# Kernel tuning notes

Hardware: AMD Instinct MI355X
Metric: run time of the kernel (lower is better)

The kernel has to match this reference:

```python
import jax, jax.numpy as jnp
import numpy as np

N, E, G = 8000, 32000, 256   # nodes, edges, graphs
F, H = 680, 10               # in-features, GAT heads
HF = F * H                   # 6800


def setup_inputs() -> dict:
    key = jax.random.key(0)
    ks = jax.random.split(key, 12)
    s = lambda i, shape, sc: (jax.random.normal(ks[i], shape, jnp.float32) * sc)
    x = jax.random.normal(ks[0], (N, F), jnp.float32)
    edge_index = jax.random.randint(ks[1], (2, E), 0, N)
    batch = jnp.arange(N) // (N // G)   # contiguous, every graph non-empty
    return dict(
        x=x, edge_index=edge_index, batch=batch,
        W_gat=s(2, (F, HF), 0.05), a_src=s(3, (H, F), 0.05), a_dst=s(4, (H, F), 0.05),
        b_gat=jnp.zeros((HF,), jnp.float32),
        W_gcn=s(5, (HF, HF), 0.01), b_gcn=jnp.zeros((HF,), jnp.float32),
        W1=s(6, (2 * HF, 512), 0.02), b1=jnp.zeros((512,), jnp.float32),
        W2=s(7, (512, 128), 0.05), b2=jnp.zeros((128,), jnp.float32),
        W3=s(8, (128, 64), 0.05), b3=jnp.zeros((64,), jnp.float32),
    )


def _self_loops(edge_index):
    loop = jnp.arange(N)
    return (jnp.concatenate([edge_index[0], loop]),
            jnp.concatenate([edge_index[1], loop]))


def _gat(x, src, dst, W, a_s, a_d, b):
    xh = (x @ W).reshape(N, H, F)                          # [N,H,F]
    al_s = jnp.einsum('nhf,hf->nh', xh, a_s)               # src attention logits
    al_d = jnp.einsum('nhf,hf->nh', xh, a_d)
    e = jax.nn.leaky_relu(al_s[src] + al_d[dst], 0.2)      # [Etot,H]
    m = jax.ops.segment_max(e, dst, num_segments=N)        # segment softmax over dst
    ex = jnp.exp(e - m[dst])
    z = jax.ops.segment_sum(ex, dst, num_segments=N)
    alpha = ex / (z[dst] + 1e-16)
    out = jax.ops.segment_sum(alpha[:, :, None] * xh[src], dst, num_segments=N)
    return out.reshape(N, HF) + b                          # concat heads + bias


def _gcn(x, src, dst, W, b):
    deg = jax.ops.segment_sum(jnp.ones_like(dst, jnp.float32), dst, num_segments=N)
    dinv = jax.lax.rsqrt(deg)                              # deg>=1 due to self-loops
    norm = dinv[src] * dinv[dst]
    xw = x @ W
    return jax.ops.segment_sum(norm[:, None] * xw[src], dst, num_segments=N) + b


def reference(x, edge_index, batch, W_gat, a_src, a_dst, b_gat, W_gcn, b_gcn,
              W1, b1, W2, b2, W3, b3):
    src, dst = _self_loops(edge_index)
    h = jax.nn.relu(_gat(x, src, dst, W_gat, a_src, a_dst, b_gat))  # dropout = id (eval)
    h = jax.nn.relu(_gcn(h, src, dst, W_gcn, b_gcn))
    gmp = jax.ops.segment_max(h, batch, num_segments=G)
    cnt = jax.ops.segment_sum(jnp.ones((N,), jnp.float32), batch, num_segments=G)
    gap = jax.ops.segment_sum(h, batch, num_segments=G) / cnt[:, None]
    g = jnp.concatenate([gmp, gap], axis=1)                # [G, 2*HF]
    g = jax.nn.relu(g @ W1 + b1)
    g = g @ W2 + b2
    return g @ W3 + b3                                     # [G, 64]
```

## Files before the change

kernel.cpp:

```cpp
#include <hip/hip_runtime.h>
#include <cstdint>
#include <cstddef>

#define DEVFN static __device__ __forceinline__

typedef __attribute__((ext_vector_type(8))) short short8;
typedef __attribute__((ext_vector_type(4))) float f32x4;

constexpr int NN  = 8000;
constexpr int NE  = 32000;
constexpr int ET  = NE + NN;
constexpr int NG  = 256;
constexpr int F   = 680;
constexpr int NH  = 10;
constexpr int HF  = 6800;

constexpr int MP   = 8192;
constexpr int KP1  = 704;
constexpr int NP   = 6912;
constexpr int KP2  = 6848;
constexpr int KM1P = 13632;

DEVFN unsigned short f2bf(float f) {
  unsigned u = __float_as_uint(f);
  u += 0x7fffu + ((u >> 16) & 1u);
  return (unsigned short)(u >> 16);
}
DEVFN float bf2f(unsigned short b) { return __uint_as_float(((unsigned)b) << 16); }

DEVFN int perm64(int k, int r) {
  return (((k >> 3) ^ (r & 7)) << 3) | (k & 7);
}

DEVFN void gload16(const void* g, void* l) {
  __builtin_amdgcn_global_load_lds(
      (const __attribute__((address_space(1))) unsigned int*)g,
      (__attribute__((address_space(3))) unsigned int*)l, 16, 0, 0);
}

DEVFN f32x4 mfma_16x16x32_bf16(short8 a, short8 b, f32x4 c) {
  asm("v_mfma_f32_16x16x32_bf16 %0, %1, %2, %0" : "+v"(c) : "v"(a), "v"(b));
  return c;
}

template<int OUT_MODE, bool BIAS, bool RELU>
__global__ __launch_bounds__(512, 2) void gemm256(
    const unsigned short* __restrict__ A, const unsigned short* __restrict__ BT,
    void* __restrict__ C, const float* __restrict__ bias,
    int K, int cstride, int nvalid, int Mt, int KC) {
  __shared__ alignas(16) char Lds[131072];
  const int tid = threadIdx.x;
  const int wave = tid >> 6, lane = tid & 63;
  const int wm = wave >> 2, wn = wave & 3;
  const int g4 = lane >> 4, l15 = lane & 15;
  const int xorc = l15 & 7;
  const int brow = (wn & 1) * 64;

  const int nwg = gridDim.x, orig = blockIdx.x;
  const int qx = nwg >> 3, r8 = nwg & 7;
  const int xcd = orig & 7, loc = orig >> 3;
  const int wg = (xcd < r8 ? xcd * (qx + 1) : r8 * (qx + 1) + (xcd - r8) * qx) + loc;
  const int bm = wg % Mt, bn = wg / Mt;

  const int NTt = K >> 6;
  const int kb = blockIdx.z * KC;
  const int NT = min(KC, NTt - kb);
  const unsigned short* Ag = A + (size_t)bm * 256 * K + (size_t)kb * 64;
  const unsigned short* Bg = BT + (size_t)bn * 256 * K + (size_t)kb * 64;

  const int srow = tid >> 3;
  const int schk = (tid & 7) * 8;

  auto stageHalf = [&](const unsigned short* G, int t, int op, int h) {
    char* base = Lds + ((((t & 1) << 2) | (op << 1) | h) << 14) + (wave << 10);
    const unsigned short* src = G + (size_t)(h * 128 + srow) * K + (size_t)t * 64 + schk;
    gload16(src, base);
    gload16(src + (size_t)64 * K, base + 8192);
  };

  const char* Ab0 = Lds + (((0 << 2) | (0 << 1) | wm) << 14);
  const char* Ab1 = Lds + (((1 << 2) | (0 << 1) | wm) << 14);
  const char* Bb0 = Lds + (((0 << 2) | (1 << 1) | (wn >> 1)) << 14);
  const char* Bb1 = Lds + (((1 << 2) | (1 << 1) | (wn >> 1)) << 14);

  f32x4 acc[8][4];
#pragma unroll
  for (int i = 0; i < 8; i++)
#pragma unroll
    for (int j = 0; j < 4; j++) acc[i][j] = (f32x4){0.f, 0.f, 0.f, 0.f};

  short8 aR[4][2], b0[2][2], b1[2][2];

#define READ_A(BASE, QM) do {                                                   \
  _Pragma("unroll") for (int i2 = 0; i2 < 4; ++i2)                              \
  _Pragma("unroll") for (int ks = 0; ks < 2; ++ks)                              \
    aR[i2][ks] = *(const short8*)((BASE) + ((QM) * 64 + i2 * 16 + l15) * 128    \
                                  + ((((ks << 2) | g4) ^ xorc) << 4));          \
} while (0)

#define READ_B(BASE, QN, DST) do {                                              \
  _Pragma("unroll") for (int j2 = 0; j2 < 2; ++j2)                              \
  _Pragma("unroll") for (int ks = 0; ks < 2; ++ks)                              \
    DST[j2][ks] = *(const short8*)((BASE) + (brow + (QN) * 32 + j2 * 16 + l15) * 128 \
                                   + ((((ks << 2) | g4) ^ xorc) << 4));         \
} while (0)

#define MMAQ(QM, QN, BREG) do {                                                 \
  _Pragma("unroll") for (int i2 = 0; i2 < 4; ++i2)                              \
  _Pragma("unroll") for (int j2 = 0; j2 < 2; ++j2)                              \
  _Pragma("unroll") for (int ks = 0; ks < 2; ++ks)                              \
    acc[(QM) * 4 + i2][(QN) * 2 + j2] =                                         \
        mfma_16x16x32_bf16(aR[i2][ks], BREG[j2][ks], acc[(QM) * 4 + i2][(QN) * 2 + j2]); \
} while (0)

  if (NT > 0) {
    stageHalf(Ag, 0, 0, 0); stageHalf(Ag, 0, 0, 1);
    stageHalf(Bg, 0, 1, 0); stageHalf(Bg, 0, 1, 1);
  }
  if (NT > 1) {
    stageHalf(Ag, 1, 0, 0); stageHalf(Ag, 1, 0, 1);
    stageHalf(Bg, 1, 1, 0); stageHalf(Bg, 1, 1, 1);
    asm volatile("s_waitcnt vmcnt(8)" ::: "memory");
  } else {
    asm volatile("s_waitcnt vmcnt(0)" ::: "memory");
  }
  __builtin_amdgcn_s_barrier();

  for (int t = 0; t < NT; ++t) {
    const char* Ac = (t & 1) ? Ab1 : Ab0;
    const char* Bc = (t & 1) ? Bb1 : Bb0;
    const bool pf = (t + 2 < NT);

    READ_A(Ac, 0);
    READ_B(Bc, 0, b0);
    __builtin_amdgcn_s_barrier();
    asm volatile("s_waitcnt lgkmcnt(0)" ::: "memory");
    __builtin_amdgcn_s_setprio(1);
    MMAQ(0, 0, b0);
    __builtin_amdgcn_s_setprio(0);
    __builtin_amdgcn_s_barrier();

    READ_B(Bc, 1, b1);
    __builtin_amdgcn_s_barrier();
    asm volatile("s_waitcnt lgkmcnt(0)" ::: "memory");
    __builtin_amdgcn_s_setprio(1);
    MMAQ(0, 1, b1);
    __builtin_amdgcn_s_setprio(0);
    __builtin_amdgcn_s_barrier();

    READ_A(Ac, 1);
    if (pf) { stageHalf(Bg, t + 2, 1, 0); stageHalf(Bg, t + 2, 1, 1); }
    __builtin_amdgcn_s_barrier();
    asm volatile("s_waitcnt lgkmcnt(0)" ::: "memory");
    __builtin_amdgcn_s_setprio(1);
    MMAQ(1, 1, b1);
    __builtin_amdgcn_s_setprio(0);
    __builtin_amdgcn_s_barrier();

    if (pf) {
      stageHalf(Ag, t + 2, 0, 0); stageHalf(Ag, t + 2, 0, 1);
      asm volatile("s_waitcnt vmcnt(8)" ::: "memory");
    } else {
      asm volatile("s_waitcnt vmcnt(0)" ::: "memory");
    }
    __builtin_amdgcn_s_barrier();
    __builtin_amdgcn_s_setprio(1);
    MMAQ(1, 0, b0);
    __builtin_amdgcn_s_setprio(0);
    __builtin_amdgcn_s_barrier();
  }

#undef READ_A
#undef READ_B
#undef MMAQ

  const int m0 = bm * 256 + wm * 128;
  const int n0 = bn * 256 + wn * 64;
  const int rb = g4 * 4;
#pragma unroll
  for (int i = 0; i < 8; i++) {
#pragma unroll
    for (int j = 0; j < 4; j++) {
      int c = n0 + j * 16 + l15;
      if (c >= nvalid) continue;
      float bv = BIAS ? bias[c] : 0.f;
#pragma unroll
      for (int tt = 0; tt < 4; tt++) {
        int r = m0 + i * 16 + rb + tt;
        float v = acc[i][j][tt] + bv;
        if (RELU) v = fmaxf(v, 0.f);
        if (OUT_MODE == 0) {
          ((float*)C)[(size_t)r * cstride + c] = v;
        } else if (OUT_MODE == 1) {
          ((unsigned short*)C)[(size_t)r * cstride + c] = f2bf(v);
        } else if (OUT_MODE == 2) {
          int pos = (c & ~63) + perm64(c & 63, r);
          ((unsigned short*)C)[(size_t)r * cstride + pos] = f2bf(v);
        } else {
          ((float*)C)[(size_t)blockIdx.z * (Mt * 256) * cstride + (size_t)r * cstride + c] = v;
        }
      }
    }
  }
}

template<bool RELU>
__global__ void finish_kernel(const float* __restrict__ acc, const float* __restrict__ bias,
                              unsigned short* __restrict__ out, int S, int M, int N) {
  int idx = blockIdx.x * 256 + threadIdx.x;
  if (idx >= M * N) return;
  int r = idx / N, c = idx - r * N;
  float s = bias[c];
  for (int k = 0; k < S; k++) s += acc[(size_t)k * M * N + (size_t)r * N + c];
  if (RELU) s = fmaxf(s, 0.f);
  out[(size_t)r * N + (c & ~63) + perm64(c & 63, r)] = f2bf(s);
}

__global__ void conv_x_kernel(const float* __restrict__ x, unsigned short* __restrict__ out) {
  int idx = blockIdx.x * 256 + threadIdx.x;
  constexpr int GR = KP1 / 4;
  if (idx >= MP * GR) return;
  int row = idx / GR, k = (idx - row * GR) * 4;
  unsigned short v[4] = {0, 0, 0, 0};
  if (row < NN && k < F) {
    const float* p = x + (size_t)row * F + k;
    v[0] = f2bf(p[0]); v[1] = f2bf(p[1]); v[2] = f2bf(p[2]); v[3] = f2bf(p[3]);
  }
  int pos = (k & ~63) + perm64(k & 63, row);
  uint2 pk;
  pk.x = (unsigned)v[0] | ((unsigned)v[1] << 16);
  pk.y = (unsigned)v[2] | ((unsigned)v[3] << 16);
  *(uint2*)&out[(size_t)row * KP1 + pos] = pk;
}

__global__ void convT_kernel(const float* __restrict__ in, unsigned short* __restrict__ out,
                             int K, int N, int KPad, int NPad) {
  __shared__ float tile[32][33];
  int n0 = blockIdx.x * 32, k0 = blockIdx.y * 32;
  int tx = threadIdx.x, ty = threadIdx.y;
#pragma unroll
  for (int i = 0; i < 4; i++) {
    int k = k0 + ty + i * 8, n = n0 + tx;
    tile[ty + i * 8][tx] = (k < K && n < N) ? in[(size_t)k * N + n] : 0.f;
  }
  __syncthreads();
#pragma unroll
  for (int i = 0; i < 4; i++) {
    int n = n0 + ty + i * 8, k = k0 + tx;
    if (n < NPad && k < KPad) {
      int pos = (k & ~63) + perm64(k & 63, n);
      out[(size_t)n * KPad + pos] = f2bf(tile[tx][ty + i * 8]);
    }
  }
}

__global__ void logits_kernel(const unsigned short* __restrict__ xh,
                              const float* __restrict__ a_src, const float* __restrict__ a_dst,
                              float* __restrict__ al_s, float* __restrict__ al_d) {
  int wid = blockIdx.x * 4 + (threadIdx.x >> 6);
  int lane = threadIdx.x & 63;
  int n = wid / NH, h = wid - n * NH;
  if (n >= NN) return;
  const unsigned short* row = xh + (size_t)n * NP + h * F;
  const float* as = a_src + h * F;
  const float* ad = a_dst + h * F;
  float ss = 0.f, sd = 0.f;
  for (int f0 = lane; f0 < F; f0 += 64) {
    float v = bf2f(row[f0]);
    ss += v * as[f0]; sd += v * ad[f0];
  }
#pragma unroll
  for (int o = 32; o > 0; o >>= 1) { ss += __shfl_down(ss, o); sd += __shfl_down(sd, o); }
  if (lane == 0) { al_s[wid] = ss; al_d[wid] = sd; }
}

__global__ void edge_count_kernel(const int* __restrict__ ei, int* __restrict__ deg) {
  int e = blockIdx.x * 256 + threadIdx.x;
  if (e >= ET) return;
  int d = (e < NE) ? ei[NE + e] : (e - NE);
  atomicAdd(&deg[d], 1);
}

__global__ void scan_kernel(const int* __restrict__ deg, int* __restrict__ rs,
                            int* __restrict__ cursor) {
  __shared__ int part[1024];
  int t = threadIdx.x;
  int base = t * 8, s = 0, loc[8];
#pragma unroll
  for (int i = 0; i < 8; i++) { loc[i] = s; int idx = base + i; s += (idx < NN) ? deg[idx] : 0; }
  part[t] = s;
  __syncthreads();
  for (int off = 1; off < 1024; off <<= 1) {
    int v = (t >= off) ? part[t - off] : 0;
    __syncthreads();
    part[t] += v;
    __syncthreads();
  }
  int pre = (t > 0) ? part[t - 1] : 0;
#pragma unroll
  for (int i = 0; i < 8; i++) {
    int idx = base + i;
    if (idx <= NN) { rs[idx] = pre + loc[i]; cursor[idx] = pre + loc[i]; }
  }
}

__global__ void edge_fill_kernel(const int* __restrict__ ei, int* __restrict__ cursor,
                                 int* __restrict__ eidx) {
  int e = blockIdx.x * 256 + threadIdx.x;
  if (e >= ET) return;
  int d = (e < NE) ? ei[NE + e] : (e - NE);
  int pos = atomicAdd(&cursor[d], 1);
  eidx[pos] = e;
}

__global__ void dinv_kernel(const int* __restrict__ deg, float* __restrict__ dinv) {
  int n = blockIdx.x * 256 + threadIdx.x;
  if (n < NN) dinv[n] = rsqrtf((float)max(deg[n], 1));
}

__global__ void alpha_kernel(const int* __restrict__ ei, const int* __restrict__ rs,
                             const int* __restrict__ eidx, const float* __restrict__ al_s,
                             const float* __restrict__ al_d, float* __restrict__ alpha) {
  int w = blockIdx.x * 256 + threadIdx.x;
  if (w >= NN * NH) return;
  int n = w / NH, h = w - n * NH;
  int s0 = rs[n], s1 = rs[n + 1];
  float ad = al_d[w];
  float m = -3.0e38f;
  for (int i = s0; i < s1; i++) {
    int e = eidx[i]; int s = (e < NE) ? ei[e] : (e - NE);
    float x = al_s[s * NH + h] + ad;
    x = (x > 0.f) ? x : 0.2f * x;
    m = fmaxf(m, x);
  }
  float z = 0.f;
  for (int i = s0; i < s1; i++) {
    int e = eidx[i]; int s = (e < NE) ? ei[e] : (e - NE);
    float x = al_s[s * NH + h] + ad;
    x = (x > 0.f) ? x : 0.2f * x;
    float ex = __expf(x - m);
    alpha[(size_t)i * NH + h] = ex;
    z += ex;
  }
  float inv = 1.f / (z + 1e-16f);
  for (int i = s0; i < s1; i++) alpha[(size_t)i * NH + h] *= inv;
}

__global__ void gat_agg_kernel(const unsigned short* __restrict__ xh, const int* __restrict__ ei,
                               const int* __restrict__ rs, const int* __restrict__ eidx,
                               const float* __restrict__ alpha, const float* __restrict__ bgat,
                               unsigned short* __restrict__ hbf) {
  int n = blockIdx.x, t = threadIdx.x;
  int s0 = rs[n], s1 = rs[n + 1];
  for (int c4 = t; c4 < KP2 / 4; c4 += 256) {
    int c = c4 * 4;
    int pos = (c & ~63) + perm64(c & 63, n);
    if (c >= HF) {
      *(uint2*)&hbf[(size_t)n * KP2 + pos] = make_uint2(0u, 0u);
      continue;
    }
    int h = c / F;
    float a0 = 0.f, a1 = 0.f, a2 = 0.f, a3 = 0.f;
    for (int i = s0; i < s1; i++) {
      int e = eidx[i]; int s = (e < NE) ? ei[e] : (e - NE);
      float al = alpha[(size_t)i * NH + h];
      uint2 r = *(const uint2*)&xh[(size_t)s * NP + c];
      a0 += al * bf2f((unsigned short)(r.x & 0xffff));
      a1 += al * bf2f((unsigned short)(r.x >> 16));
      a2 += al * bf2f((unsigned short)(r.y & 0xffff));
      a3 += al * bf2f((unsigned short)(r.y >> 16));
    }
    a0 = fmaxf(a0 + bgat[c], 0.f);     a1 = fmaxf(a1 + bgat[c + 1], 0.f);
    a2 = fmaxf(a2 + bgat[c + 2], 0.f); a3 = fmaxf(a3 + bgat[c + 3], 0.f);
    uint2 pk;
    pk.x = (unsigned)f2bf(a0) | ((unsigned)f2bf(a1) << 16);
    pk.y = (unsigned)f2bf(a2) | ((unsigned)f2bf(a3) << 16);
    *(uint2*)&hbf[(size_t)n * KP2 + pos] = pk;
  }
}

__global__ void gcn_agg_kernel(const unsigned short* __restrict__ xw, const int* __restrict__ ei,
                               const int* __restrict__ rs, const int* __restrict__ eidx,
                               const float* __restrict__ dinv, const float* __restrict__ bgcn,
                               unsigned short* __restrict__ h2) {
  int n = blockIdx.x, t = threadIdx.x;
  int s0 = rs[n], s1 = rs[n + 1];
  float dn = dinv[n];
  for (int c4 = t; c4 < HF / 4; c4 += 256) {
    int c = c4 * 4;
    float a0 = 0.f, a1 = 0.f, a2 = 0.f, a3 = 0.f;
    for (int i = s0; i < s1; i++) {
      int e = eidx[i]; int s = (e < NE) ? ei[e] : (e - NE);
      float w = dinv[s] * dn;
      uint2 r = *(const uint2*)&xw[(size_t)s * NP + c];
      a0 += w * bf2f((unsigned short)(r.x & 0xffff));
      a1 += w * bf2f((unsigned short)(r.x >> 16));
      a2 += w * bf2f((unsigned short)(r.y & 0xffff));
      a3 += w * bf2f((unsigned short)(r.y >> 16));
    }
    a0 = fmaxf(a0 + bgcn[c], 0.f);     a1 = fmaxf(a1 + bgcn[c + 1], 0.f);
    a2 = fmaxf(a2 + bgcn[c + 2], 0.f); a3 = fmaxf(a3 + bgcn[c + 3], 0.f);
    uint2 pk;
    pk.x = (unsigned)f2bf(a0) | ((unsigned)f2bf(a1) << 16);
    pk.y = (unsigned)f2bf(a2) | ((unsigned)f2bf(a3) << 16);
    *(uint2*)&h2[(size_t)n * KP2 + c] = pk;
  }
}

__global__ void pool_init_kernel(int* gstart, int* gend, int* gcnt) {
  int g = threadIdx.x;
  gstart[g] = 0x7fffffff; gend[g] = 0; gcnt[g] = 0;
}
__global__ void pool_scan_kernel(const int* __restrict__ batch, int* gstart, int* gend, int* gcnt) {
  int n = blockIdx.x * 256 + threadIdx.x;
  if (n >= NN) return;
  int b = batch[n];
  if (b >= 0 && b < NG) {
    atomicMin(&gstart[b], n);
    atomicMax(&gend[b], n + 1);
    atomicAdd(&gcnt[b], 1);
  }
}
__global__ void pool_kernel(const unsigned short* __restrict__ h2, const int* __restrict__ batch,
                            const int* __restrict__ gstart, const int* __restrict__ gend,
                            const int* __restrict__ gcnt, unsigned short* __restrict__ gbf) {
  int g = blockIdx.x, t = threadIdx.x;
  int s = gstart[g], e = gend[g];
  float cnt = (float)max(gcnt[g], 1);
  for (int c = t; c < HF; c += 256) {
    float vmax = -3.0e38f, vsum = 0.f;
    for (int n = s; n < e; n++) {
      if (batch[n] != g) continue;
      float v = bf2f(h2[(size_t)n * KP2 + c]);
      vmax = fmaxf(vmax, v);
      vsum += v;
    }
    int c1 = c, c2 = HF + c;
    gbf[(size_t)g * KM1P + (c1 & ~63) + perm64(c1 & 63, g)] = f2bf(vmax);
    gbf[(size_t)g * KM1P + (c2 & ~63) + perm64(c2 & 63, g)] = f2bf(vsum / cnt);
  }
}

extern "C" void kernel_launch(void* const* d_in, const int* in_sizes, int n_in,
                              void* d_out, int out_size, void* d_ws, size_t ws_size,
                              hipStream_t stream) {
  (void)in_sizes; (void)n_in; (void)out_size; (void)ws_size;
  const float* x     = (const float*)d_in[0];
  const int*   ei    = (const int*)d_in[1];
  const int*   batch = (const int*)d_in[2];
  const float* W_gat = (const float*)d_in[3];
  const float* a_src = (const float*)d_in[4];
  const float* a_dst = (const float*)d_in[5];
  const float* b_gat = (const float*)d_in[6];
  const float* W_gcn = (const float*)d_in[7];
  const float* b_gcn = (const float*)d_in[8];
  const float* W1    = (const float*)d_in[9];
  const float* b1    = (const float*)d_in[10];
  const float* W2    = (const float*)d_in[11];
  const float* b2    = (const float*)d_in[12];
  const float* W3    = (const float*)d_in[13];
  const float* b3    = (const float*)d_in[14];
  float* out = (float*)d_out;

  char* ws = (char*)d_ws;
  size_t off = 0;
  auto alloc = [&](size_t bytes) -> void* {
    void* p = ws + off;
    off += (bytes + 255) & ~(size_t)255;
    return p;
  };
  unsigned short* bufA  = (unsigned short*)alloc((size_t)MP * NP * 2);
  unsigned short* bufB  = (unsigned short*)alloc((size_t)MP * KP2 * 2);
  unsigned short* wgcnT = (unsigned short*)alloc((size_t)NP * KP2 * 2);
  unsigned short* xbf   = (unsigned short*)alloc((size_t)MP * KP1 * 2);
  unsigned short* wgatT = (unsigned short*)alloc((size_t)NP * KP1 * 2);
  unsigned short* w1T   = (unsigned short*)alloc((size_t)512 * KM1P * 2);
  unsigned short* gbf   = (unsigned short*)alloc((size_t)NG * KM1P * 2);
  unsigned short* w2T   = (unsigned short*)alloc((size_t)256 * 512 * 2);
  unsigned short* w3T   = (unsigned short*)alloc((size_t)256 * 128 * 2);
  unsigned short* g1bf  = (unsigned short*)alloc((size_t)NG * 512 * 2);
  unsigned short* g2bf  = (unsigned short*)alloc((size_t)NG * 128 * 2);
  float* accf  = (float*)alloc((size_t)8 * 256 * 512 * 4);
  float* al_s  = (float*)alloc((size_t)NN * NH * 4);
  float* al_d  = (float*)alloc((size_t)NN * NH * 4);
  float* alpha = (float*)alloc((size_t)ET * NH * 4);
  float* dinv  = (float*)alloc((size_t)NN * 4);
  int* deg    = (int*)alloc((size_t)NN * 4);
  int* rs     = (int*)alloc((size_t)(NN + 1) * 4);
  int* cursor = (int*)alloc((size_t)(NN + 1) * 4);
  int* eidx   = (int*)alloc((size_t)ET * 4);
  int* gstart = (int*)alloc((size_t)NG * 4);
  int* gend   = (int*)alloc((size_t)NG * 4);
  int* gcnt   = (int*)alloc((size_t)NG * 4);

  constexpr int MT = MP / 256;
  constexpr int NT_ = NP / 256;

  conv_x_kernel<<<(MP * (KP1 / 4)) / 256, 256, 0, stream>>>(x, xbf);
  convT_kernel<<<dim3(NP / 32, KP1 / 32), dim3(32, 8), 0, stream>>>(W_gat, wgatT, F, HF, KP1, NP);
  convT_kernel<<<dim3(NP / 32, KP2 / 32), dim3(32, 8), 0, stream>>>(W_gcn, wgcnT, HF, HF, KP2, NP);
  convT_kernel<<<dim3(512 / 32, KM1P / 32), dim3(32, 8), 0, stream>>>(W1, w1T, 2 * HF, 512, KM1P, 512);
  convT_kernel<<<dim3(256 / 32, 512 / 32), dim3(32, 8), 0, stream>>>(W2, w2T, 512, 128, 512, 256);
  convT_kernel<<<dim3(256 / 32, 128 / 32), dim3(32, 8), 0, stream>>>(W3, w3T, 128, 64, 128, 256);
  hipMemsetAsync(deg, 0, (size_t)NN * 4, stream);
  hipMemsetAsync((char*)bufB + (size_t)NN * KP2 * 2, 0, (size_t)(MP - NN) * KP2 * 2, stream);
  hipMemsetAsync(gbf, 0, (size_t)NG * KM1P * 2, stream);

  gemm256<1, false, false><<<dim3(MT * NT_, 1, 1), 512, 0, stream>>>(
      xbf, wgatT, bufA, nullptr, KP1, NP, NP, MT, KP1 / 64);

  logits_kernel<<<(NN * NH) / 4, 256, 0, stream>>>(bufA, a_src, a_dst, al_s, al_d);

  edge_count_kernel<<<(ET + 255) / 256, 256, 0, stream>>>(ei, deg);
  scan_kernel<<<1, 1024, 0, stream>>>(deg, rs, cursor);
  edge_fill_kernel<<<(ET + 255) / 256, 256, 0, stream>>>(ei, cursor, eidx);
  dinv_kernel<<<(NN + 255) / 256, 256, 0, stream>>>(deg, dinv);

  alpha_kernel<<<(NN * NH + 255) / 256, 256, 0, stream>>>(ei, rs, eidx, al_s, al_d, alpha);

  gat_agg_kernel<<<NN, 256, 0, stream>>>(bufA, ei, rs, eidx, alpha, b_gat, bufB);

  gemm256<1, false, false><<<dim3(MT * NT_, 1, 1), 512, 0, stream>>>(
      bufB, wgcnT, bufA, nullptr, KP2, NP, NP, MT, KP2 / 64);

  gcn_agg_kernel<<<NN, 256, 0, stream>>>(bufA, ei, rs, eidx, dinv, b_gcn, bufB);

  pool_init_kernel<<<1, 256, 0, stream>>>(gstart, gend, gcnt);
  pool_scan_kernel<<<(NN + 255) / 256, 256, 0, stream>>>(batch, gstart, gend, gcnt);
  pool_kernel<<<NG, 256, 0, stream>>>(bufB, batch, gstart, gend, gcnt, gbf);

  gemm256<3, false, false><<<dim3(1 * 2, 1, 8), 512, 0, stream>>>(
      gbf, w1T, accf, nullptr, KM1P, 512, 512, 1, 27);
  finish_kernel<true><<<(256 * 512) / 256, 256, 0, stream>>>(accf, b1, g1bf, 8, 256, 512);

  gemm256<3, false, false><<<dim3(1, 1, 4), 512, 0, stream>>>(
      g1bf, w2T, accf, nullptr, 512, 128, 128, 1, 2);
  finish_kernel<false><<<(256 * 128) / 256, 256, 0, stream>>>(accf, b2, g2bf, 4, 256, 128);

  gemm256<0, true, false><<<dim3(1, 1, 1), 512, 0, stream>>>(
      g2bf, w3T, out, b3, 128, 64, 64, 1, 2);
}
```

Before: 1.688 ms.

## Cut per-iteration barriers in GEMM main loop and add XCD-aware tile mapping

Restructures the bf16 GEMM K-loop from eight barriers and explicit lgkmcnt waits per iteration down to three. Prefetches of the next B and A tiles are issued right after the barrier that follows the last reads of that buffer, so global loads overlap the remaining MFMA quads. It also replaces the generic work-group remap with a fixed swizzle for the two large GEMMs, so each XCD handles one N-column of tiles across all M tiles. Out-of-range tiles exit early. The costs are a hard-coded grid shape (32x32) tied to these matrix sizes, and less barrier-enforced lockstep between waves, which could change LDS contention.

Measured after the change: 1.623 ms. -3.8%, faster.

```diff
diff --git a/kernel.cpp b/kernel.cpp
--- a/kernel.cpp
+++ b/kernel.cpp
@@ -43,7 +43,7 @@
   return c;
 }
 
-template<int OUT_MODE, bool BIAS, bool RELU>
+template<int OUT_MODE, bool BIAS, bool RELU, bool SWZ>
 __global__ __launch_bounds__(512, 2) void gemm256(
     const unsigned short* __restrict__ A, const unsigned short* __restrict__ BT,
     void* __restrict__ C, const float* __restrict__ bias,
@@ -56,11 +56,18 @@
   const int xorc = l15 & 7;
   const int brow = (wn & 1) * 64;
 
-  const int nwg = gridDim.x, orig = blockIdx.x;
-  const int qx = nwg >> 3, r8 = nwg & 7;
-  const int xcd = orig & 7, loc = orig >> 3;
-  const int wg = (xcd < r8 ? xcd * (qx + 1) : r8 * (qx + 1) + (xcd - r8) * qx) + loc;
-  const int bm = wg % Mt, bn = wg / Mt;
+  int bm, bn;
+  if (SWZ) {
+    const int xcd = blockIdx.x & 7;
+    const int j = blockIdx.x >> 3;
+    bm = j & 31;
+    bn = (j >> 5) * 8 + xcd;
+    const int Nt = (nvalid + 255) >> 8;
+    if (bn >= Nt) return;
+  } else {
+    bm = blockIdx.x % Mt;
+    bn = blockIdx.x / Mt;
+  }
 
   const int NTt = K >> 6;
   const int kb = blockIdx.z * KC;
@@ -124,7 +131,7 @@
   } else {
     asm volatile("s_waitcnt vmcnt(0)" ::: "memory");
   }
-  __builtin_amdgcn_s_barrier();
+  asm volatile("s_barrier" ::: "memory");
 
   for (int t = 0; t < NT; ++t) {
     const char* Ac = (t & 1) ? Ab1 : Ab0;
@@ -133,41 +140,33 @@
 
     READ_A(Ac, 0);
     READ_B(Bc, 0, b0);
-    __builtin_amdgcn_s_barrier();
-    asm volatile("s_waitcnt lgkmcnt(0)" ::: "memory");
     __builtin_amdgcn_s_setprio(1);
     MMAQ(0, 0, b0);
     __builtin_amdgcn_s_setprio(0);
-    __builtin_amdgcn_s_barrier();
 
     READ_B(Bc, 1, b1);
-    __builtin_amdgcn_s_barrier();
-    asm volatile("s_waitcnt lgkmcnt(0)" ::: "memory");
     __builtin_amdgcn_s_setprio(1);
     MMAQ(0, 1, b1);
     __builtin_amdgcn_s_setprio(0);
-    __builtin_amdgcn_s_barrier();
+
+    asm volatile("s_barrier" ::: "memory");
+    if (pf) { stageHalf(Bg, t + 2, 1, 0); stageHalf(Bg, t + 2, 1, 1); }
 
     READ_A(Ac, 1);
-    if (pf) { stageHalf(Bg, t + 2, 1, 0); stageHalf(Bg, t + 2, 1, 1); }
-    __builtin_amdgcn_s_barrier();
-    asm volatile("s_waitcnt lgkmcnt(0)" ::: "memory");
     __builtin_amdgcn_s_setprio(1);
     MMAQ(1, 1, b1);
     __builtin_amdgcn_s_setprio(0);
-    __builtin_amdgcn_s_barrier();
-
-    if (pf) {
-      stageHalf(Ag, t + 2, 0, 0); stageHalf(Ag, t + 2, 0, 1);
-      asm volatile("s_waitcnt vmcnt(8)" ::: "memory");
-    } else {
-      asm volatile("s_waitcnt vmcnt(0)" ::: "memory");
-    }
-    __builtin_amdgcn_s_barrier();
+
+    asm volatile("s_barrier" ::: "memory");
+    if (pf) { stageHalf(Ag, t + 2, 0, 0); stageHalf(Ag, t + 2, 0, 1); }
+
     __builtin_amdgcn_s_setprio(1);
     MMAQ(1, 0, b0);
     __builtin_amdgcn_s_setprio(0);
-    __builtin_amdgcn_s_barrier();
+
+    if (pf) asm volatile("s_waitcnt vmcnt(8)" ::: "memory");
+    else    asm volatile("s_waitcnt vmcnt(0)" ::: "memory");
+    asm volatile("s_barrier" ::: "memory");
   }
 
 #undef READ_A
@@ -494,7 +493,7 @@
   int* gcnt   = (int*)alloc((size_t)NG * 4);
 
   constexpr int MT = MP / 256;
-  constexpr int NT_ = NP / 256;
+  constexpr int GRID_SWZ = 32 * 32;
 
   conv_x_kernel<<<(MP * (KP1 / 4)) / 256, 256, 0, stream>>>(x, xbf);
   convT_kernel<<<dim3(NP / 32, KP1 / 32), dim3(32, 8), 0, stream>>>(W_gat, wgatT, F, HF, KP1, NP);
@@ -506,7 +505,7 @@
   hipMemsetAsync((char*)bufB + (size_t)NN * KP2 * 2, 0, (size_t)(MP - NN) * KP2 * 2, stream);
   hipMemsetAsync(gbf, 0, (size_t)NG * KM1P * 2, stream);
 
-  gemm256<1, false, false><<<dim3(MT * NT_, 1, 1), 512, 0, stream>>>(
+  gemm256<1, false, false, true><<<dim3(GRID_SWZ, 1, 1), 512, 0, stream>>>(
       xbf, wgatT, bufA, nullptr, KP1, NP, NP, MT, KP1 / 64);
 
   logits_kernel<<<(NN * NH) / 4, 256, 0, stream>>>(bufA, a_src, a_dst, al_s, al_d);
@@ -520,7 +519,7 @@
 
   gat_agg_kernel<<<NN, 256, 0, stream>>>(bufA, ei, rs, eidx, alpha, b_gat, bufB);
 
-  gemm256<1, false, false><<<dim3(MT * NT_, 1, 1), 512, 0, stream>>>(
+  gemm256<1, false, false, true><<<dim3(GRID_SWZ, 1, 1), 512, 0, stream>>>(
       bufB, wgcnT, bufA, nullptr, KP2, NP, NP, MT, KP2 / 64);
 
   gcn_agg_kernel<<<NN, 256, 0, stream>>>(bufA, ei, rs, eidx, dinv, b_gcn, bufB);
@@ -529,14 +528,14 @@
   pool_scan_kernel<<<(NN + 255) / 256, 256, 0, stream>>>(batch, gstart, gend, gcnt);
   pool_kernel<<<NG, 256, 0, stream>>>(bufB, batch, gstart, gend, gcnt, gbf);
 
-  gemm256<3, false, false><<<dim3(1 * 2, 1, 8), 512, 0, stream>>>(
+  gemm256<3, false, false, false><<<dim3(1 * 2, 1, 8), 512, 0, stream>>>(
       gbf, w1T, accf, nullptr, KM1P, 512, 512, 1, 27);
   finish_kernel<true><<<(256 * 512) / 256, 256, 0, stream>>>(accf, b1, g1bf, 8, 256, 512);
 
-  gemm256<3, false, false><<<dim3(1, 1, 4), 512, 0, stream>>>(
+  gemm256<3, false, false, false><<<dim3(1, 1, 4), 512, 0, stream>>>(
       g1bf, w2T, accf, nullptr, 512, 128, 128, 1, 2);
   finish_kernel<false><<<(256 * 128) / 256, 256, 0, stream>>>(accf, b2, g2bf, 4, 256, 128);
 
-  gemm256<0, true, false><<<dim3(1, 1, 1), 512, 0, stream>>>(
+  gemm256<0, true, false, false><<<dim3(1, 1, 1), 512, 0, stream>>>(
       g2bf, w3T, out, b3, 128, 64, 64, 1, 2);
 }
```
